# Optimization experiments

Hardware: AMD Instinct MI355X
Metric: run time of the kernel (lower is better)

Reference implementation:

```python
import jax, jax.numpy as jnp
import numpy as np
import math

N, E = 20000, 200000
MUL = 128            # multiplicity of the 0e and 1o channels
D = MUL + 3 * MUL    # 512 = node feature dim
EDGE_ATTR = 32
HID = 32             # invariant_neurons
LOG2 = math.log(2.0)


def ssp(x):
    # ShiftedSoftPlus
    return jax.nn.softplus(x) - LOG2


def split_irreps(x):
    # x: [?, 512] -> (l=0 part [?, MUL], l=1 part [?, MUL, 3])
    return x[:, :MUL], x[:, MUL:].reshape(x.shape[0], MUL, 3)


def merge_irreps(x0, x1):
    return jnp.concatenate([x0, x1.reshape(x1.shape[0], MUL * 3)], axis=-1)


def irrep_linear(x, W0, b0, W1):
    # e3nn o3.Linear: per-irrep channel mixing; bias only on l=0
    x0, x1 = split_irreps(x)
    y0 = x0 @ W0 + b0
    y1 = jnp.einsum('nuc,uv->nvc', x1, W1)
    return merge_irreps(y0, y1)


def setup_inputs() -> dict:
    key = jax.random.key(0)
    ks = iter(jax.random.split(key, 32))

    def randn(shape, scale=1.0):
        return (scale * jax.random.normal(next(ks), shape)).astype(jnp.float32)

    inp = {
        'x': randn((N, D)),
        'edge_sh': randn((E, 4)),
        'edge_attr': jax.random.uniform(next(ks), (E, EDGE_ATTR), dtype=jnp.float32),
        'edge_index': jax.random.randint(next(ks), (2, E), 0, N, dtype=jnp.int32),
        # linear_node_pre
        'W_pre0': randn((MUL, MUL), MUL ** -0.5), 'b_pre0': jnp.zeros((MUL,), jnp.float32),
        'W_pre1': randn((MUL, MUL), MUL ** -0.5),
        # linear_node
        'W_nd0': randn((MUL, MUL), MUL ** -0.5), 'b_nd0': jnp.zeros((MUL,), jnp.float32),
        'W_nd1': randn((MUL, MUL), MUL ** -0.5),
        # NormGate fc: Linear(2*MUL,2*MUL)+SiLU+Linear(2*MUL,2*MUL)
        'W_g1': randn((2 * MUL, 2 * MUL), (2 * MUL) ** -0.5), 'b_g1': jnp.zeros((2 * MUL,), jnp.float32),
        'W_g2': randn((2 * MUL, 2 * MUL), (2 * MUL) ** -0.5), 'b_g2': jnp.zeros((2 * MUL,), jnp.float32),
        # fc_node: FullyConnectedNet([32, 32, 4*MUL], ssp) -- no biases
        'W_f1': randn((EDGE_ATTR, HID), EDGE_ATTR ** -0.5),
        'W_f2': randn((HID, 4 * MUL), HID ** -0.5),
        # layer_l0: FullyConnectedNet([3*MUL, 32, 4*MUL], ssp)
        'W_s1': randn((3 * MUL, HID), (3 * MUL) ** -0.5),
        'W_s2': randn((HID, 4 * MUL), HID ** -0.5),
        # linear_out
        'W_o0': randn((MUL, MUL), MUL ** -0.5), 'b_o0': jnp.zeros((MUL,), jnp.float32),
        'W_o1': randn((MUL, MUL), MUL ** -0.5),
    }
    return inp


def reference(x, edge_sh, edge_attr, edge_index,
              W_pre0, b_pre0, W_pre1, W_nd0, b_nd0, W_nd1,
              W_g1, b_g1, W_g2, b_g2, W_f1, W_f2, W_s1, W_s2,
              W_o0, b_o0, W_o1):
    edge_dst, edge_src = edge_index[0], edge_index[1]
    old_x = x

    # ---- s0 edge invariants: linear_node_pre + InnerProduct (uuu, /dim)
    pre = irrep_linear(x, W_pre0, b_pre0, W_pre1)
    p0, p1 = split_irreps(pre)
    pd0 = p0[edge_dst]
    ip1 = jnp.einsum('eum,eum->eu', p1[edge_dst], p1[edge_src]) / 3.0   # l=1 inner product [E, MUL]
    s0 = jnp.concatenate([pd0, pd0, ip1], axis=-1)                      # [E, 3*MUL]

    # ---- NormGate then linear_node on node features
    x0, x1 = split_irreps(x)
    n1 = jnp.sqrt(jnp.sum(x1 * x1, axis=-1) / 3.0)                      # per-irrep norm [N, MUL]
    g = jax.nn.silu(jnp.concatenate([x0, n1], -1) @ W_g1 + b_g1) @ W_g2 + b_g2
    xg = merge_irreps(g[:, :MUL], x1 * g[:, MUL:, None])
    x = irrep_linear(xg, W_nd0, b_nd0, W_nd1)
    self_x = x

    # ---- per-edge tensor-product weights (fc_node(edge_attr) * layer_l0(s0))
    w = (ssp(edge_attr @ W_f1) @ W_f2) * (ssp(s0 @ W_s1) @ W_s2)        # [E, 4*MUL]
    w1, w2, w3, w4 = jnp.split(w, 4, axis=-1)

    # ---- gather + equivariant tensor product with edge spherical harmonics (uvu paths)
    x0e, x1e = split_irreps(x[edge_src])
    sh0, sh1 = edge_sh[:, 0], edge_sh[:, 1:4]
    # paths: 0e*0e->0e, 1o*1o->0e (dot), 0e*1o->1o, 1o*0e->1o
    out0 = w1 * x0e * sh0[:, None] + w4 * (jnp.einsum('eum,em->eu', x1e, sh1) / jnp.sqrt(3.0))
    out1 = (w2[:, :, None] * x0e[:, :, None] * sh1[:, None, :]
            + w3[:, :, None] * x1e * sh0[:, None, None])
    edge_feat = merge_irreps(out0, out1)                                # [E, D]

    # ---- scatter messages back to destination nodes
    out = jax.ops.segment_sum(edge_feat, edge_dst, num_segments=old_x.shape[0])
    out = out + self_x                                                  # irrep_in == irrep_out skip
    out = irrep_linear(out, W_o0, b_o0, W_o1)
    return out + old_x                                                  # ConvNetLayer resnet
```

## Files before the change

### kernel.cpp

```cpp
#include <hip/hip_runtime.h>
#include <hip/hip_fp16.h>
#include <math.h>

#define NN 20000
#define EE 200000

__device__ __forceinline__ float sspf(float x){
    float sp = (x > 20.f) ? x : log1pf(expf(x));
    return sp - 0.69314718056f;
}

__device__ __forceinline__ void fma8(float* acc, const float* base, float w){
    const float4 a = ((const float4*)base)[0];
    const float4 b = ((const float4*)base)[1];
    acc[0]+=a.x*w; acc[1]+=a.y*w; acc[2]+=a.z*w; acc[3]+=a.w*w;
    acc[4]+=b.x*w; acc[5]+=b.y*w; acc[6]+=b.z*w; acc[7]+=b.w*w;
}

__global__ __launch_bounds__(256) void k_pre(
    const float* __restrict__ x, const float* __restrict__ Wp0,
    const float* __restrict__ bp0, const float* __restrict__ Wp1,
    const float* __restrict__ Ws1,
    float* __restrict__ p1, float* __restrict__ sdst)
{
    __shared__ float xl[512][8];
    __shared__ float p0l[8][128];
    const int tid = threadIdx.x;
    const int n0 = blockIdx.x * 8;

    for (int it = 0; it < 4; ++it){
        int idx = tid + 256*it;
        int node = idx >> 7, o4 = idx & 127;
        float4 v = ((const float4*)(x + (size_t)(n0+node)*512))[o4];
        xl[o4*4+0][node]=v.x; xl[o4*4+1][node]=v.y;
        xl[o4*4+2][node]=v.z; xl[o4*4+3][node]=v.w;
    }
    __syncthreads();

    const int j = tid;
    float acc1[8] = {0,0,0,0,0,0,0,0};
    float acc2[8] = {0,0,0,0,0,0,0,0};
    const int o2 = j + 128;
    const int v2 = o2/3, m2 = o2%3;

    if (j < 128){
        for (int u = 0; u < 128; ++u){
            float w1 = Wp0[u*128 + j];
            float w2 = Wp1[u*128 + v2];
            fma8(acc1, &xl[u][0], w1);
            fma8(acc2, &xl[128 + u*3 + m2][0], w2);
        }
        float b = bp0[j];
        #pragma unroll
        for (int n = 0; n < 8; ++n) p0l[n][j] = acc1[n] + b;
    } else {
        const int o1 = j - 128, v1 = o1/3, m1 = o1%3;
        for (int u = 0; u < 128; ++u){
            float w1 = Wp1[u*128 + v1];
            float w2 = Wp1[u*128 + v2];
            fma8(acc1, &xl[128 + u*3 + m1][0], w1);
            fma8(acc2, &xl[128 + u*3 + m2][0], w2);
        }
        #pragma unroll
        for (int n = 0; n < 8; ++n) p1[(size_t)(n0+n)*384 + (j-128)] = acc1[n];
    }
    #pragma unroll
    for (int n = 0; n < 8; ++n) p1[(size_t)(n0+n)*384 + o2] = acc2[n];
    __syncthreads();

    {
        int n = tid >> 5, h = tid & 31;
        float s = 0.f;
        for (int u = 0; u < 128; ++u){
            float wc = Ws1[u*32 + h] + Ws1[(128+u)*32 + h];
            s += p0l[n][u] * wc;
        }
        sdst[(size_t)(n0+n)*32 + h] = s;
    }
}

__global__ __launch_bounds__(256) void k_gate_nd(
    const float* __restrict__ x,
    const float* __restrict__ Wg1, const float* __restrict__ bg1,
    const float* __restrict__ Wg2, const float* __restrict__ bg2,
    const float* __restrict__ Wnd0, const float* __restrict__ bnd0,
    const float* __restrict__ Wnd1,
    float* __restrict__ self_x)
{
    __shared__ float xl[512][8];
    __shared__ float tl[256][8];
    __shared__ float hl[256][8];
    const int tid = threadIdx.x;
    const int n0 = blockIdx.x * 8;

    for (int it = 0; it < 4; ++it){
        int idx = tid + 256*it;
        int node = idx >> 7, o4 = idx & 127;
        float4 v = ((const float4*)(x + (size_t)(n0+node)*512))[o4];
        xl[o4*4+0][node]=v.x; xl[o4*4+1][node]=v.y;
        xl[o4*4+2][node]=v.z; xl[o4*4+3][node]=v.w;
    }
    __syncthreads();

    {
        int jj = tid;
        if (jj < 128){
            #pragma unroll
            for (int n = 0; n < 8; ++n) tl[jj][n] = xl[jj][n];
        } else {
            int u = jj - 128;
            #pragma unroll
            for (int n = 0; n < 8; ++n){
                float a = xl[128+u*3][n], b = xl[128+u*3+1][n], c = xl[128+u*3+2][n];
                tl[jj][n] = sqrtf((a*a + b*b + c*c) * (1.f/3.f));
            }
        }
    }
    __syncthreads();

    {
        float acc[8] = {0,0,0,0,0,0,0,0};
        for (int k = 0; k < 256; ++k){
            float w = Wg1[k*256 + tid];
            fma8(acc, &tl[k][0], w);
        }
        float b = bg1[tid];
        #pragma unroll
        for (int n = 0; n < 8; ++n){
            float v = acc[n] + b;
            hl[tid][n] = v / (1.f + expf(-v));
        }
    }
    __syncthreads();

    {
        float acc[8] = {0,0,0,0,0,0,0,0};
        for (int k = 0; k < 256; ++k){
            float w = Wg2[k*256 + tid];
            fma8(acc, &hl[k][0], w);
        }
        float b = bg2[tid];
        #pragma unroll
        for (int n = 0; n < 8; ++n) tl[tid][n] = acc[n] + b;
    }
    __syncthreads();

    {
        int jj = tid;
        if (jj < 128){
            #pragma unroll
            for (int n = 0; n < 8; ++n) xl[jj][n] = tl[jj][n];
        } else {
            int u = jj - 128;
            #pragma unroll
            for (int n = 0; n < 8; ++n){
                float g1 = tl[128+u][n];
                xl[128+u*3  ][n] *= g1;
                xl[128+u*3+1][n] *= g1;
                xl[128+u*3+2][n] *= g1;
            }
        }
    }
    __syncthreads();

    const int j = tid;
    float acc1[8] = {0,0,0,0,0,0,0,0};
    float acc2[8] = {0,0,0,0,0,0,0,0};
    const int o2 = j + 128;
    const int v2 = o2/3, m2 = o2%3;
    if (j < 128){
        for (int u = 0; u < 128; ++u){
            float w1 = Wnd0[u*128 + j];
            float w2 = Wnd1[u*128 + v2];
            fma8(acc1, &xl[u][0], w1);
            fma8(acc2, &xl[128 + u*3 + m2][0], w2);
        }
        float b = bnd0[j];
        #pragma unroll
        for (int n = 0; n < 8; ++n) self_x[(size_t)(n0+n)*512 + j] = acc1[n] + b;
    } else {
        const int o1 = j - 128, v1 = o1/3, m1 = o1%3;
        for (int u = 0; u < 128; ++u){
            float w1 = Wnd1[u*128 + v1];
            float w2 = Wnd1[u*128 + v2];
            fma8(acc1, &xl[128 + u*3 + m1][0], w1);
            fma8(acc2, &xl[128 + u*3 + m2][0], w2);
        }
        #pragma unroll
        for (int n = 0; n < 8; ++n) self_x[(size_t)(n0+n)*512 + j] = acc1[n];
    }
    #pragma unroll
    for (int n = 0; n < 8; ++n) self_x[(size_t)(n0+n)*512 + j + 256] = acc2[n];
}

__global__ __launch_bounds__(256) void k_count(
    const int* __restrict__ eidx, int* __restrict__ cnt)
{
    int e = blockIdx.x * 256 + threadIdx.x;
    if (e < EE){
        int d = eidx[e];
        if (d >= 0 && d < NN) atomicAdd(&cnt[d], 1);
    }
}

__global__ __launch_bounds__(256) void k_scan(
    const int* __restrict__ cnt, int* __restrict__ rowptr, int* __restrict__ cur)
{
    __shared__ int part[256];
    const int t = threadIdx.x;
    const int CHUNK = 79;
    const int base = t * CHUNK;
    int s = 0;
    for (int i = 0; i < CHUNK; ++i){
        int idx = base + i;
        if (idx < NN) s += cnt[idx];
    }
    part[t] = s;
    __syncthreads();
    for (int off = 1; off < 256; off <<= 1){
        int v = (t >= off) ? part[t-off] : 0;
        __syncthreads();
        part[t] += v;
        __syncthreads();
    }
    int run = (t == 0) ? 0 : part[t-1];
    for (int i = 0; i < CHUNK; ++i){
        int idx = base + i;
        if (idx < NN){
            rowptr[idx] = run;
            cur[idx]    = run;
            run += cnt[idx];
        }
    }
    if (t == 255) rowptr[NN] = run;
}

__global__ __launch_bounds__(256) void k_fill(
    const int* __restrict__ eidx, int* __restrict__ cur, int2* __restrict__ ebuf,
    int* __restrict__ dstbuf)
{
    int e = blockIdx.x * 256 + threadIdx.x;
    if (e < EE){
        int dst = eidx[e];
        int src = eidx[EE + e];
        if (dst >= 0 && dst < NN){
            int pos = atomicAdd(&cur[dst], 1);
            if (pos >= 0 && pos < EE){
                ebuf[pos] = make_int2(e, src);
                dstbuf[pos] = dst;
            }
        }
    }
}

__global__ __launch_bounds__(256) void k_edge_pre(
    const float* __restrict__ p1g, const float* __restrict__ sdst,
    const float* __restrict__ ea,
    const int2* __restrict__ ebuf, const int* __restrict__ dstbuf,
    const float* __restrict__ Wf1, const float* __restrict__ Ws1,
    float* __restrict__ fbuf, float* __restrict__ sbuf)
{
    __shared__ float p1d[8][384], p1s[8][384];
    __shared__ float eal[8][32], sdl[8][32];
    __shared__ float ip1l[8][128];
    __shared__ int eidl[8], srcl[8], dstl[8];
    const int tid = threadIdx.x;
    const long e0 = (long)blockIdx.x * 8;

    if (tid < 8){
        int2 pe = ebuf[e0 + tid];
        if (!(pe.x >= 0 && pe.x < EE)) pe.x = 0;
        if (!(pe.y >= 0 && pe.y < NN)) pe.y = 0;
        int d = dstbuf[e0 + tid];
        if (!(d >= 0 && d < NN)) d = 0;
        eidl[tid] = pe.x; srcl[tid] = pe.y; dstl[tid] = d;
    }
    __syncthreads();

    for (int e = 0; e < 8; ++e){
        int dst = dstl[e], src = srcl[e], eid = eidl[e];
        if (tid < 96)
            ((float4*)p1d[e])[tid] = ((const float4*)(p1g + (size_t)dst*384))[tid];
        else if (tid < 192)
            ((float4*)p1s[e])[tid-96] = ((const float4*)(p1g + (size_t)src*384))[tid-96];
        else if (tid < 200)
            ((float4*)eal[e])[tid-192] = ((const float4*)(ea + (size_t)eid*32))[tid-192];
        else if (tid < 208)
            ((float4*)sdl[e])[tid-200] = ((const float4*)(sdst + (size_t)dst*32))[tid-200];
    }
    __syncthreads();

    for (int it = 0; it < 4; ++it){
        int idx = tid + 256*it;
        int e = idx >> 7, u = idx & 127;
        ip1l[e][u] = (p1d[e][u*3]*p1s[e][u*3] + p1d[e][u*3+1]*p1s[e][u*3+1]
                    + p1d[e][u*3+2]*p1s[e][u*3+2]) * (1.f/3.f);
    }
    __syncthreads();

    {
        int e = tid >> 5, h = tid & 31;
        float f = 0.f;
        for (int k = 0; k < 32; ++k) f += eal[e][k] * Wf1[k*32 + h];
        float s = sdl[e][h];
        for (int u = 0; u < 128; ++u) s += ip1l[e][u] * Ws1[(256+u)*32 + h];
        fbuf[(e0+e)*32 + h] = sspf(f);
        sbuf[(e0+e)*32 + h] = sspf(s);
    }
}

__global__ __launch_bounds__(256) void k_edge_one(
    const float* __restrict__ fbuf, const float* __restrict__ sbuf,
    const float* __restrict__ self_x, const float* __restrict__ esh,
    const int2* __restrict__ ebuf, const int* __restrict__ dstbuf,
    const float* __restrict__ Wf2, const float* __restrict__ Ws2,
    float* __restrict__ out)
{
    __shared__ float fbl[64][32];
    __shared__ float sbl[64][32];
    __shared__ float shl[64][4];
    __shared__ int   srcl[64], dl[64];

    const int tid = threadIdx.x;
    const int c   = tid >> 1;
    const int h   = tid & 1;
    const long e0 = (long)blockIdx.x * 64;
    const float IS3 = 0.57735026919f;

    float wfA[32], wfB[32], wsA[32], wsB[32];
    {
        const int qA = 2*h*128 + c, qB = (2*h+1)*128 + c;
        #pragma unroll
        for (int k = 0; k < 32; ++k){
            wfA[k] = Wf2[(size_t)k*512 + qA];
            wfB[k] = Wf2[(size_t)k*512 + qB];
            wsA[k] = Ws2[(size_t)k*512 + qA];
            wsB[k] = Ws2[(size_t)k*512 + qB];
        }
    }

    if (tid < 64){
        int2 pe = ebuf[e0 + tid];
        if (!(pe.x >= 0 && pe.x < EE)) pe.x = 0;
        if (!(pe.y >= 0 && pe.y < NN)) pe.y = 0;
        int d = dstbuf[e0 + tid];
        if (!(d >= 0 && d < NN)) d = 0;
        srcl[tid] = pe.y; dl[tid] = d;
        ((float4*)shl)[tid] = ((const float4*)esh)[pe.x];
    }
    {
        const float4* fsrc = (const float4*)(fbuf + (size_t)e0*32);
        const float4* ssrc = (const float4*)(sbuf + (size_t)e0*32);
        ((float4*)fbl)[tid]       = fsrc[tid];
        ((float4*)fbl)[tid + 256] = fsrc[tid + 256];
        ((float4*)sbl)[tid]       = ssrc[tid];
        ((float4*)sbl)[tid + 256] = ssrc[tid + 256];
    }
    __syncthreads();

    const int dprev = (blockIdx.x == 0)    ? -1 : dstbuf[e0 - 1];
    const int dnext = (e0 + 64 < EE)       ? dstbuf[e0 + 64] : -1;

    float a0 = 0.f, a1 = 0.f;
    int sstart = 0;

    const float* sx0 = self_x + (size_t)srcl[0]*512;
    float px = sx0[c];
    float p0 = sx0[128 + 3*c];
    float p1v = sx0[128 + 3*c + 1];
    float p2 = sx0[128 + 3*c + 2];

    for (int e = 0; e < 64; ++e){
        const float x0c = px, v0 = p0, v1 = p1v, v2 = p2;
        if (e < 63){
            const float* sx = self_x + (size_t)srcl[e+1]*512;
            px  = sx[c];
            p0  = sx[128 + 3*c];
            p1v = sx[128 + 3*c + 1];
            p2  = sx[128 + 3*c + 2];
        }

        float FA = 0.f, FB = 0.f, SA = 0.f, SB = 0.f;
        #pragma unroll
        for (int k4 = 0; k4 < 8; ++k4){
            float4 fb4 = *(const float4*)&fbl[e][k4*4];
            float4 sb4 = *(const float4*)&sbl[e][k4*4];
            FA += fb4.x*wfA[k4*4+0]; FB += fb4.x*wfB[k4*4+0];
            SA += sb4.x*wsA[k4*4+0]; SB += sb4.x*wsB[k4*4+0];
            FA += fb4.y*wfA[k4*4+1]; FB += fb4.y*wfB[k4*4+1];
            SA += sb4.y*wsA[k4*4+1]; SB += sb4.y*wsB[k4*4+1];
            FA += fb4.z*wfA[k4*4+2]; FB += fb4.z*wfB[k4*4+2];
            SA += sb4.z*wsA[k4*4+2]; SB += sb4.z*wsB[k4*4+2];
            FA += fb4.w*wfA[k4*4+3]; FB += fb4.w*wfB[k4*4+3];
            SA += sb4.w*wsA[k4*4+3]; SB += sb4.w*wsB[k4*4+3];
        }
        const float wA = FA*SA, wB = FB*SB;
        const float oA = __shfl_xor(wA, 1);
        const float oB = __shfl_xor(wB, 1);
        const float w1 = h ? oA : wA;
        const float w2 = h ? oB : wB;
        const float w3 = h ? wA : oA;
        const float w4 = h ? wB : oB;

        const float4 sh = *(const float4*)&shl[e][0];
        const int dste = dl[e];

        const float dot = v0*sh.y + v1*sh.z + v2*sh.w;
        const float caw = h ? w2 : w1;
        const float cf  = h ? sh.z : sh.x;
        const float cbw = h ? w3 : w4*IS3;
        const float cg  = h ? v1*sh.x : dot;
        a0 += caw*x0c*cf + cbw*cg;
        const float shm = h ? sh.w : sh.y;
        const float vm  = h ? v2 : v0;
        a1 += w2*x0c*shm + w3*vm*sh.x;

        if (e == 63 || dl[e+1] != dste){
            const bool openL = (sstart == 0) && (dprev == dste);
            const bool openR = (e == 63) && (dnext == dste);
            float* orow = out + (size_t)dste*512;
            const int pos0 = h ? (128 + 3*c + 1) : c;
            const int pos1 = h ? (128 + 3*c + 2) : (128 + 3*c);
            if (openL || openR){
                atomicAdd(orow + pos0, a0);
                atomicAdd(orow + pos1, a1);
            } else {
                orow[pos0] = a0;
                orow[pos1] = a1;
            }
            a0 = 0.f; a1 = 0.f; sstart = e + 1;
        }
    }
}

__global__ __launch_bounds__(256) void k_post(
    const float* __restrict__ self_x, const float* __restrict__ x,
    const float* __restrict__ Wo0, const float* __restrict__ bo0,
    const float* __restrict__ Wo1,
    float* __restrict__ out)
{
    __shared__ float tl[512][8];
    const int tid = threadIdx.x;
    const int n0 = blockIdx.x * 8;

    for (int it = 0; it < 4; ++it){
        int idx = tid + 256*it;
        int node = idx >> 7, o4 = idx & 127;
        float4 a = ((const float4*)(out    + (size_t)(n0+node)*512))[o4];
        float4 b = ((const float4*)(self_x + (size_t)(n0+node)*512))[o4];
        tl[o4*4+0][node]=a.x+b.x; tl[o4*4+1][node]=a.y+b.y;
        tl[o4*4+2][node]=a.z+b.z; tl[o4*4+3][node]=a.w+b.w;
    }
    __syncthreads();

    const int j = tid;
    float acc1[8] = {0,0,0,0,0,0,0,0};
    float acc2[8] = {0,0,0,0,0,0,0,0};
    const int o2 = j + 128;
    const int v2 = o2/3, m2 = o2%3;
    if (j < 128){
        for (int u = 0; u < 128; ++u){
            float w1 = Wo0[u*128 + j];
            float w2 = Wo1[u*128 + v2];
            fma8(acc1, &tl[u][0], w1);
            fma8(acc2, &tl[128 + u*3 + m2][0], w2);
        }
        float b = bo0[j];
        #pragma unroll
        for (int n = 0; n < 8; ++n)
            out[(size_t)(n0+n)*512 + j] = acc1[n] + b + x[(size_t)(n0+n)*512 + j];
    } else {
        const int o1 = j - 128, v1 = o1/3, m1 = o1%3;
        for (int u = 0; u < 128; ++u){
            float w1 = Wo1[u*128 + v1];
            float w2 = Wo1[u*128 + v2];
            fma8(acc1, &tl[128 + u*3 + m1][0], w1);
            fma8(acc2, &tl[128 + u*3 + m2][0], w2);
        }
        #pragma unroll
        for (int n = 0; n < 8; ++n)
            out[(size_t)(n0+n)*512 + j] = acc1[n] + x[(size_t)(n0+n)*512 + j];
    }
    #pragma unroll
    for (int n = 0; n < 8; ++n)
        out[(size_t)(n0+n)*512 + j + 256] = acc2[n] + x[(size_t)(n0+n)*512 + j + 256];
}

extern "C" void kernel_launch(void* const* d_in, const int* in_sizes, int n_in,
                              void* d_out, int out_size, void* d_ws, size_t ws_size,
                              hipStream_t stream)
{
    const float* x    = (const float*)d_in[0];
    const float* esh  = (const float*)d_in[1];
    const float* ea   = (const float*)d_in[2];
    const int*   eidx = (const int*)  d_in[3];
    const float* Wp0  = (const float*)d_in[4];
    const float* bp0  = (const float*)d_in[5];
    const float* Wp1  = (const float*)d_in[6];
    const float* Wnd0 = (const float*)d_in[7];
    const float* bnd0 = (const float*)d_in[8];
    const float* Wnd1 = (const float*)d_in[9];
    const float* Wg1  = (const float*)d_in[10];
    const float* bg1  = (const float*)d_in[11];
    const float* Wg2  = (const float*)d_in[12];
    const float* bg2  = (const float*)d_in[13];
    const float* Wf1  = (const float*)d_in[14];
    const float* Wf2  = (const float*)d_in[15];
    const float* Ws1  = (const float*)d_in[16];
    const float* Ws2  = (const float*)d_in[17];
    const float* Wo0  = (const float*)d_in[18];
    const float* bo0  = (const float*)d_in[19];
    const float* Wo1  = (const float*)d_in[20];

    float* out  = (float*)d_out;
    float* ws   = (float*)d_ws;
    float* p1   = ws;
    float* sdst = p1   + (size_t)NN*384;
    float* sfx  = sdst + (size_t)NN*32;
    float* fbuf = sfx  + (size_t)NN*512;
    float* sbuf = fbuf + (size_t)EE*32;

    int*  dcnt  = (int*)d_out;
    int*  dcur  = dcnt + NN;
    int*  drow  = dcur + NN;
    int2* debuf = (int2*)(drow + NN + 4);
    int*  ddst  = (int*)(debuf + EE);

    hipMemsetAsync(dcnt, 0, (size_t)NN*sizeof(int), stream);
    k_count <<<(EE+255)/256, 256, 0, stream>>>(eidx, dcnt);
    k_scan  <<<1, 256, 0, stream>>>(dcnt, drow, dcur);
    k_fill  <<<(EE+255)/256, 256, 0, stream>>>(eidx, dcur, debuf, ddst);

    k_pre     <<<NN/8, 256, 0, stream>>>(x, Wp0, bp0, Wp1, Ws1, p1, sdst);
    k_gate_nd <<<NN/8, 256, 0, stream>>>(x, Wg1, bg1, Wg2, bg2, Wnd0, bnd0, Wnd1, sfx);
    k_edge_pre<<<EE/8, 256, 0, stream>>>(p1, sdst, ea, debuf, ddst, Wf1, Ws1,
                                         fbuf, sbuf);

    int2* ebuf2   = (int2*)ws;
    int*  dstbuf2 = (int*)ws + (size_t)2*EE;
    hipMemcpyAsync(ws, debuf, (size_t)3*EE*sizeof(int),
                   hipMemcpyDeviceToDevice, stream);
    hipMemsetAsync(out, 0, (size_t)NN*512*sizeof(float), stream);

    k_edge_one<<<EE/64, 256, 0, stream>>>(fbuf, sbuf, sfx, esh, ebuf2, dstbuf2,
                                          Wf2, Ws2, out);

    k_post    <<<NN/8, 256, 0, stream>>>(sfx, x, Wo0, bo0, Wo1, out);
}
```

Baseline: 1.036 ms.

## Restructure edge_pre kernel to one wavefront per edge with register dot products

The per-edge pre-kernel now assigns one 64-lane wavefront to each edge instead of staging 8 edges of p1 rows in shared memory. Each lane loads 6 floats of the dst and src rows directly into registers, computes two l=1 inner products, and only the 128-element result goes to LDS. The two 32-wide matvecs are split across the half-waves and combined with a shuffle. This cuts LDS footprint and barriers and spreads the small matvecs over more threads, at the cost of twice as many blocks and uncoalesced float2 loads from global memory.

```diff
diff --git a/kernel.cpp b/kernel.cpp
--- a/kernel.cpp
+++ b/kernel.cpp
@@ -253,59 +253,62 @@
     }
 }
 
-__global__ __launch_bounds__(256) void k_edge_pre(
+__global__ __launch_bounds__(256, 4) void k_edge_pre(
     const float* __restrict__ p1g, const float* __restrict__ sdst,
     const float* __restrict__ ea,
     const int2* __restrict__ ebuf, const int* __restrict__ dstbuf,
     const float* __restrict__ Wf1, const float* __restrict__ Ws1,
     float* __restrict__ fbuf, float* __restrict__ sbuf)
 {
-    __shared__ float p1d[8][384], p1s[8][384];
-    __shared__ float eal[8][32], sdl[8][32];
-    __shared__ float ip1l[8][128];
-    __shared__ int eidl[8], srcl[8], dstl[8];
-    const int tid = threadIdx.x;
-    const long e0 = (long)blockIdx.x * 8;
-
-    if (tid < 8){
-        int2 pe = ebuf[e0 + tid];
-        if (!(pe.x >= 0 && pe.x < EE)) pe.x = 0;
-        if (!(pe.y >= 0 && pe.y < NN)) pe.y = 0;
-        int d = dstbuf[e0 + tid];
-        if (!(d >= 0 && d < NN)) d = 0;
-        eidl[tid] = pe.x; srcl[tid] = pe.y; dstl[tid] = d;
-    }
-    __syncthreads();
-
-    for (int e = 0; e < 8; ++e){
-        int dst = dstl[e], src = srcl[e], eid = eidl[e];
-        if (tid < 96)
-            ((float4*)p1d[e])[tid] = ((const float4*)(p1g + (size_t)dst*384))[tid];
-        else if (tid < 192)
-            ((float4*)p1s[e])[tid-96] = ((const float4*)(p1g + (size_t)src*384))[tid-96];
-        else if (tid < 200)
-            ((float4*)eal[e])[tid-192] = ((const float4*)(ea + (size_t)eid*32))[tid-192];
-        else if (tid < 208)
-            ((float4*)sdl[e])[tid-200] = ((const float4*)(sdst + (size_t)dst*32))[tid-200];
-    }
-    __syncthreads();
-
-    for (int it = 0; it < 4; ++it){
-        int idx = tid + 256*it;
-        int e = idx >> 7, u = idx & 127;
-        ip1l[e][u] = (p1d[e][u*3]*p1s[e][u*3] + p1d[e][u*3+1]*p1s[e][u*3+1]
-                    + p1d[e][u*3+2]*p1s[e][u*3+2]) * (1.f/3.f);
-    }
-    __syncthreads();
-
-    {
-        int e = tid >> 5, h = tid & 31;
-        float f = 0.f;
-        for (int k = 0; k < 32; ++k) f += eal[e][k] * Wf1[k*32 + h];
-        float s = sdl[e][h];
-        for (int u = 0; u < 128; ++u) s += ip1l[e][u] * Ws1[(256+u)*32 + h];
-        fbuf[(e0+e)*32 + h] = sspf(f);
-        sbuf[(e0+e)*32 + h] = sspf(s);
+    __shared__ float ipw[4][128];
+    const int tid  = threadIdx.x;
+    const int wv   = tid >> 6, lane = tid & 63;
+    const long e   = (long)blockIdx.x * 4 + wv;
+
+    int2 pe = ebuf[e];
+    if (!(pe.x >= 0 && pe.x < EE)) pe.x = 0;
+    if (!(pe.y >= 0 && pe.y < NN)) pe.y = 0;
+    int dst = dstbuf[e];
+    if (!(dst >= 0 && dst < NN)) dst = 0;
+
+    const float* pd = p1g + (size_t)dst*384 + lane*6;
+    const float* ps = p1g + (size_t)pe.y*384 + lane*6;
+    const float2 d01 = *(const float2*)(pd);
+    const float2 d23 = *(const float2*)(pd+2);
+    const float2 d45 = *(const float2*)(pd+4);
+    const float2 s01 = *(const float2*)(ps);
+    const float2 s23 = *(const float2*)(ps+2);
+    const float2 s45 = *(const float2*)(ps+4);
+    const float ipa = (d01.x*s01.x + d01.y*s01.y + d23.x*s23.x) * (1.f/3.f);
+    const float ipb = (d23.y*s23.y + d45.x*s45.x + d45.y*s45.y) * (1.f/3.f);
+    *(float2*)&ipw[wv][lane*2] = make_float2(ipa, ipb);
+
+    const int h = lane & 31;
+    const float sdv = sdst[(size_t)dst*32 + h];
+
+    __syncthreads();
+
+    const int uh = (lane >> 5) * 64;
+    float sA = 0.f, sB = 0.f;
+    #pragma unroll 8
+    for (int uu = 0; uu < 64; uu += 2){
+        sA += ipw[wv][uh+uu]   * Ws1[(256+uh+uu)*32 + h];
+        sB += ipw[wv][uh+uu+1] * Ws1[(257+uh+uu)*32 + h];
+    }
+    float s = sA + sB;
+    s += __shfl_xor(s, 32);
+
+    const int kh = (lane >> 5) * 16;
+    const float* ear = ea + (size_t)pe.x*32 + kh;
+    float f = 0.f;
+    #pragma unroll 8
+    for (int kk = 0; kk < 16; ++kk)
+        f += ear[kk] * Wf1[(kh+kk)*32 + h];
+    f += __shfl_xor(f, 32);
+
+    if (lane < 32){
+        sbuf[e*32 + h] = sspf(s + sdv);
+        fbuf[e*32 + h] = sspf(f);
     }
 }
 
@@ -533,7 +536,7 @@
 
     k_pre     <<<NN/8, 256, 0, stream>>>(x, Wp0, bp0, Wp1, Ws1, p1, sdst);
     k_gate_nd <<<NN/8, 256, 0, stream>>>(x, Wg1, bg1, Wg2, bg2, Wnd0, bnd0, Wnd1, sfx);
-    k_edge_pre<<<EE/8, 256, 0, stream>>>(p1, sdst, ea, debuf, ddst, Wf1, Ws1,
+    k_edge_pre<<<EE/4, 256, 0, stream>>>(p1, sdst, ea, debuf, ddst, Wf1, Ws1,
                                          fbuf, sbuf);
 
     int2* ebuf2   = (int2*)ws;
```

Measured after the change: 947.8 us. -8.5%, faster.
